# Optimization experiments

Hardware: AMD Instinct MI355X
Metric: run time of the kernel (lower is better)

The kernel has to match this reference:

```python
import jax, jax.numpy as jnp
import numpy as np

B, T_H, T_F = 8192, 128, 125
MOTION_DIM, H = 6, 128


def setup_inputs() -> dict:
    key = jax.random.key(0)
    ks = jax.random.split(key, 24)
    s = 1.0 / np.sqrt(H)  # torch LSTM/Linear default init scale

    def p(k, shape):
        return jax.random.uniform(k, shape, jnp.float32, -s, s)

    inp = {"hist": jax.random.normal(ks[0], (B, T_H, MOTION_DIM), jnp.float32)}
    i = 1
    for pre, in0 in (("enc", MOTION_DIM), ("dec", 2)):
        for l, ind in enumerate((in0, H)):
            inp[f"{pre}_Wih{l}"] = p(ks[i], (4 * H, ind)); i += 1
            inp[f"{pre}_Whh{l}"] = p(ks[i], (4 * H, H)); i += 1
            inp[f"{pre}_bih{l}"] = p(ks[i], (4 * H,)); i += 1
            inp[f"{pre}_bhh{l}"] = p(ks[i], (4 * H,)); i += 1
    inp["head_W1"] = p(ks[i], (128, H)); i += 1
    inp["head_b1"] = p(ks[i], (128,)); i += 1
    inp["head_W2"] = p(ks[i], (2, 128)); i += 1
    inp["head_b2"] = p(ks[i], (2,)); i += 1
    return inp


def _cell(x, h, c, Wih, Whh, bih, bhh):
    # PyTorch LSTM gate order: i, f, g, o
    gates = x @ Wih.T + h @ Whh.T + (bih + bhh)
    i, f, g, o = jnp.split(gates, 4, axis=-1)
    c = jax.nn.sigmoid(f) * c + jax.nn.sigmoid(i) * jnp.tanh(g)
    h = jax.nn.sigmoid(o) * jnpp_tanh(c) if False else jax.nn.sigmoid(o) * jnp.tanh(c)
    return h, c


def reference(hist,
              enc_Wih0, enc_Whh0, enc_bih0, enc_bhh0,
              enc_Wih1, enc_Whh1, enc_bih1, enc_bhh1,
              dec_Wih0, dec_Whh0, dec_bih0, dec_bhh0,
              dec_Wih1, dec_Whh1, dec_bih1, dec_bhh1,
              head_W1, head_b1, head_W2, head_b2):
    b = hist.shape[0]
    z = jnp.zeros((b, H), hist.dtype)

    # ---- encoder: 2-layer LSTM over hist, keep only final (h, c) ----
    def enc_step(carry, x_t):
        h0, c0, h1, c1 = carry
        h0, c0 = _cell(x_t, h0, c0, enc_Wih0, enc_Whh0, enc_bih0, enc_bhh0)
        h1, c1 = _cell(h0, h1, c1, enc_Wih1, enc_Whh1, enc_bih1, enc_bhh1)
        return (h0, c0, h1, c1), None

    (h0, c0, h1, c1), _ = jax.lax.scan(
        enc_step, (z, z, z, z), jnp.swapaxes(hist, 0, 1))  # [T_h, B, 6]

    last_pos = hist[:, -1, :2]

    def dec_step(carry, _):
        h0, c0, h1, c1, x = carry
        h0, c0 = _cell(x, h0, c0, dec_Wih0, dec_Whh0, dec_bih0, dec_bhh0)
        h1, c1 = _cell(h0, h1, c1, dec_Wih1, dec_Whh1, dec_bih1, dec_bhh1)
        nxt = jax.nn.relu(h1 @ head_W1.T + head_b1) @ head_W2.T + head_b2
        return (h0, c0, h1, c1, nxt), nxt

    _, preds = jax.lax.scan(dec_step, (h0, c0, h1, c1, last_pos), None,
                            length=T_F)
    return jnp.swapaxes(preds, 0, 1)  # [B, T_f, 2]
```

## Files before the change

### kernel.cpp

```cpp
#include <hip/hip_runtime.h>


typedef _Float16 f16;
typedef _Float16 f16x4 __attribute__((ext_vector_type(4)));
typedef _Float16 f16x8 __attribute__((ext_vector_type(8)));
typedef float    f32x4 __attribute__((ext_vector_type(4)));

#define MFMA16(a,b,c) __builtin_amdgcn_mfma_f32_16x16x32_f16((a),(b),(c),0,0,0)

#define BM 32
#define NBLK 256
#define PACE_TGT 32

#define HOFF_E0 0
#define HOFF_E1 81920
#define HOFF_D0 212992
#define HOFF_D1 294912
#define HOFF_H  425984
#define H_TOTAL 442368
#define FOFF    221184
#define FB_E0 0
#define FB_E1 512
#define FB_D0 1024
#define FB_D1 1536
#define FB_H1 2048
#define FB_W2 2176
#define FB_B2 2432
#define F_TOTAL 2434
#define BAR_F   2560
#define BAR_BYTES 8192

#define HS 140
#define XS 36
#define O1S 133

#define HBUF 4480
#define XBUF 1152
#define L_H0 0
#define L_H1 8960
#define L_XH 17920
#define L_XL 20224
#define L_HALVES 22528

__device__ __forceinline__ float fsig(float x){ return 1.0f/(1.0f+__expf(-x)); }
__device__ __forceinline__ float ftanh(float x){
  float a = fabsf(x);
  float e = __expf(-2.0f*a);
  float t = (1.0f-e)/(1.0f+e);
  return x < 0.0f ? -t : t;
}

__device__ __forceinline__ void grid_pace(unsigned* __restrict__ bar, int idx, int g, int tid){
  __syncthreads();
  if (tid == 0){
    unsigned* p = &bar[idx*8 + g];
    __hip_atomic_fetch_add(p, 1u, __ATOMIC_RELAXED, __HIP_MEMORY_SCOPE_AGENT);
    while (__hip_atomic_load(p, __ATOMIC_RELAXED, __HIP_MEMORY_SCOPE_AGENT) < (unsigned)PACE_TGT)
      __builtin_amdgcn_s_sleep(1);
  }
  __syncthreads();
}

template<int STRIDE>
__device__ __forceinline__ f16x8 load_afrag(const f16* buf, int m, int kc, int lane){
  const f16* p = buf + (m*16 + (lane&15))*STRIDE + kc + ((lane>>4)<<2);
  f16x4 lo = *(const f16x4*)p;
  f16x4 hi = *(const f16x4*)(p+16);
  return __builtin_shufflevector(lo, hi, 0,1,2,3,4,5,6,7);
}

__device__ __forceinline__ void init_acc(f32x4 acc[2][4],
                                         const float* __restrict__ bias, int wv, int lane){
#pragma unroll
  for (int i=0;i<4;++i){
    float bv = bias[i*128 + wv*16 + (lane&15)];
    f32x4 b4 = {bv,bv,bv,bv};
    acc[0][i]=b4; acc[1][i]=b4;
  }
}

template<int KT, int SPLIT, int SB, bool CLO>
__device__ __forceinline__ void gemm2(f32x4 acc[2][4],
    const f16x8* __restrict__ Bp,
    const f16* __restrict__ Ah,
    const f16* __restrict__ Ch, const f16* __restrict__ Cl,
    int wv, int lane)
{
  f16x8 Bc[4], Bn[4];
#pragma unroll
  for (int i=0;i<4;++i) Bc[i] = Bp[(i*8 + wv)*64 + lane];
#pragma unroll
  for (int kt=0; kt<KT; ++kt){
    if (kt+1 < KT){
#pragma unroll
      for (int i=0;i<4;++i) Bn[i] = Bp[((kt+1)*32 + i*8 + wv)*64 + lane];
    }
    if (kt < SPLIT){
      int kc = kt*32;
      f16x8 a0h = load_afrag<HS>(Ah, 0, kc, lane);
      f16x8 a1h = load_afrag<HS>(Ah, 1, kc, lane);
#pragma unroll
      for (int i=0;i<4;++i){
        acc[0][i] = MFMA16(a0h, Bc[i], acc[0][i]);
        acc[1][i] = MFMA16(a1h, Bc[i], acc[1][i]);
      }
    } else {
      int kc = (kt-SPLIT)*32;
      f16x8 c0h = load_afrag<SB>(Ch, 0, kc, lane);
      f16x8 c1h = load_afrag<SB>(Ch, 1, kc, lane);
#pragma unroll
      for (int i=0;i<4;++i){
        acc[0][i] = MFMA16(c0h, Bc[i], acc[0][i]);
        acc[1][i] = MFMA16(c1h, Bc[i], acc[1][i]);
      }
      if (CLO){
        f16x8 c0l = load_afrag<SB>(Cl, 0, kc, lane);
        f16x8 c1l = load_afrag<SB>(Cl, 1, kc, lane);
#pragma unroll
        for (int i=0;i<4;++i){
          acc[0][i] = MFMA16(c0l, Bc[i], acc[0][i]);
          acc[1][i] = MFMA16(c1l, Bc[i], acc[1][i]);
        }
      }
    }
#pragma unroll
    for (int i=0;i<4;++i) Bc[i] = Bn[i];
  }
}

__device__ __forceinline__ void lstm_update_m(f32x4 acc[2][4], float cr[2][4],
    f16* __restrict__ Dh, int wv, int lane)
{
  const int unit = wv*16 + (lane&15);
  const int rg   = (lane>>4)<<2;
#pragma unroll
  for (int mt=0;mt<2;++mt)
#pragma unroll
  for (int r=0;r<4;++r){
    float iv = fsig(acc[mt][0][r]);
    float fv = fsig(acc[mt][1][r]);
    float gv = ftanh(acc[mt][2][r]);
    float ov = fsig(acc[mt][3][r]);
    float cn = fv*cr[mt][r] + iv*gv;
    cr[mt][r] = cn;
    float h = ov*ftanh(cn);
    Dh[(mt*16 + rg + r)*HS + unit] = (f16)h;
  }
}

__global__ void __launch_bounds__(512, 2)
lstm_main(const float* __restrict__ hist, float* __restrict__ ws,
          float* __restrict__ out)
{
  const f16* wh = (const f16*)ws;
  const float* wf = ws + FOFF;
  unsigned* bar = (unsigned*)(ws + FOFF + BAR_F);
  const f16x8* BE0 = (const f16x8*)(wh + HOFF_E0);
  const f16x8* BE1 = (const f16x8*)(wh + HOFF_E1);
  const f16x8* BD0 = (const f16x8*)(wh + HOFF_D0);
  const f16x8* BD1 = (const f16x8*)(wh + HOFF_D1);
  const f16x8* BH  = (const f16x8*)(wh + HOFF_H);

  __shared__ __align__(16) f16 smem[L_HALVES];
  __shared__ __align__(16) float o1buf[32*O1S];

  const int tid  = threadIdx.x;
  const int wv   = tid >> 6;
  const int lane = tid & 63;
  const int b0   = blockIdx.x * BM;
  const int g    = blockIdx.x & 7;
  const int lidx = lane & 15;

  for (int i = tid; i < L_HALVES; i += 512) smem[i] = (f16)0.f;
  float c0r[2][4] = {{0,0,0,0},{0,0,0,0}};
  float c1r[2][4] = {{0,0,0,0},{0,0,0,0}};
  f32x4 acc[2][4];

  const int lr = tid/6, ld = tid - (tid/6)*6;

  __syncthreads();
  if (tid < 192){
    float v = hist[(b0+lr)*768 + ld];
    f16 hv = (f16)v;
    smem[L_XH + XBUF + lr*XS + ld] = hv;
    smem[L_XL + XBUF + lr*XS + ld] = (f16)(v - (float)hv);
  }
  __syncthreads();

  for (int t=0; t<128; ++t){
    const int c  = t & 1;
    const int hw = c*HBUF, hr = (c^1)*HBUF;
    const int xw = c*XBUF, xr = (c^1)*XBUF;

    init_acc(acc, wf + FB_E0, wv, lane);
    gemm2<5,4,XS,true>(acc, BE0,
                       smem + L_H0 + hr,
                       smem + L_XH + xr, smem + L_XL + xr, wv, lane);
    if (t < 127 && tid < 192){
      float v = hist[(b0+lr)*768 + (t+1)*6 + ld];
      f16 hv = (f16)v;
      smem[L_XH + xw + lr*XS + ld] = hv;
      smem[L_XL + xw + lr*XS + ld] = (f16)(v - (float)hv);
    }
    lstm_update_m(acc, c0r, smem + L_H0 + hw, wv, lane);
    __syncthreads();

    init_acc(acc, wf + FB_E1, wv, lane);
    gemm2<8,4,HS,false>(acc, BE1,
                        smem + L_H0 + hw,
                        smem + L_H1 + hr, smem + L_H1 + hr, wv, lane);
    lstm_update_m(acc, c1r, smem + L_H1 + hw, wv, lane);
    grid_pace(bar, t, g, tid);
  }

  if (tid < 64){
    int r = tid>>1, j = tid&1;
    float v = hist[(b0+r)*768 + 762 + j];
    f16 hv = (f16)v;
    smem[L_XH + XBUF + r*XS + j] = hv;
    smem[L_XL + XBUF + r*XS + j] = (f16)(v - (float)hv);
  }
  __syncthreads();

  for (int t=0; t<125; ++t){
    const int c  = t & 1;
    const int hw = c*HBUF, hr = (c^1)*HBUF;
    const int xw = c*XBUF, xr = (c^1)*XBUF;

    init_acc(acc, wf + FB_D0, wv, lane);
    gemm2<5,4,XS,true>(acc, BD0,
                       smem + L_H0 + hr,
                       smem + L_XH + xr, smem + L_XL + xr, wv, lane);
    lstm_update_m(acc, c0r, smem + L_H0 + hw, wv, lane);
    __syncthreads();

    init_acc(acc, wf + FB_D1, wv, lane);
    gemm2<8,4,HS,false>(acc, BD1,
                        smem + L_H0 + hw,
                        smem + L_H1 + hr, smem + L_H1 + hr, wv, lane);
    lstm_update_m(acc, c1r, smem + L_H1 + hw, wv, lane);
    __syncthreads();

    {
      const f16* h1wH = smem + L_H1 + hw;
      float bH1 = wf[FB_H1 + wv*16 + lidx];
      f32x4 ha0 = {bH1,bH1,bH1,bH1};
      f32x4 ha1 = ha0;
#pragma unroll
      for (int kt=0;kt<4;++kt){
        f16x8 Wc = BH[(kt*8 + wv)*64 + lane];
        int kc = kt*32;
        f16x8 a0h = load_afrag<HS>(h1wH, 0, kc, lane);
        f16x8 a1h = load_afrag<HS>(h1wH, 1, kc, lane);
        ha0 = MFMA16(a0h, Wc, ha0);
        ha1 = MFMA16(a1h, Wc, ha1);
      }
#pragma unroll
      for (int r=0;r<4;++r){
        float v0 = ha0[r]; v0 = v0 > 0.f ? v0 : 0.f;
        float v1 = ha1[r]; v1 = v1 > 0.f ? v1 : 0.f;
        int rr = ((lane>>4)<<2) + r;
        o1buf[rr*O1S      + wv*16 + lidx] = v0;
        o1buf[(16+rr)*O1S + wv*16 + lidx] = v1;
      }
    }
    __syncthreads();

    if (tid < 64){
      int r = tid>>1, j = tid&1;
      const float* op = o1buf + r*O1S;
      const float* w2 = wf + FB_W2 + j;
      float s0=0.f,s1=0.f,s2=0.f,s3=0.f;
#pragma unroll
      for (int k=0;k<128;k+=4){
        s0 = fmaf(op[k],   w2[2*k],   s0);
        s1 = fmaf(op[k+1], w2[2*k+2], s1);
        s2 = fmaf(op[k+2], w2[2*k+4], s2);
        s3 = fmaf(op[k+3], w2[2*k+6], s3);
      }
      float pred = wf[FB_B2 + j] + ((s0+s1)+(s2+s3));
      out[(b0+r)*250 + t*2 + j] = pred;
      f16 ph = (f16)pred;
      smem[L_XH + xw + r*XS + j] = ph;
      smem[L_XL + xw + r*XS + j] = (f16)(pred - (float)ph);
    }
    grid_pace(bar, 128 + t, g, tid);
  }
}

__global__ void setup_kernel(
    const float* __restrict__ eWih0, const float* __restrict__ eWhh0,
    const float* __restrict__ ebih0, const float* __restrict__ ebhh0,
    const float* __restrict__ eWih1, const float* __restrict__ eWhh1,
    const float* __restrict__ ebih1, const float* __restrict__ ebhh1,
    const float* __restrict__ dWih0, const float* __restrict__ dWhh0,
    const float* __restrict__ dbih0, const float* __restrict__ dbhh0,
    const float* __restrict__ dWih1, const float* __restrict__ dWhh1,
    const float* __restrict__ dbih1, const float* __restrict__ dbhh1,
    const float* __restrict__ W1, const float* __restrict__ b1,
    const float* __restrict__ W2, const float* __restrict__ b2,
    float* __restrict__ ws)
{
  int i = blockIdx.x*256 + threadIdx.x;
  if (i < H_TOTAL){
    f16* whp = (f16*)ws;
    const float *Wa, *Wb; int ka, kb, off; bool head = false;
    if      (i < HOFF_E1){ off=HOFF_E0; Wa=eWhh0; ka=128; Wb=eWih0; kb=6; }
    else if (i < HOFF_D0){ off=HOFF_E1; Wa=eWih1; ka=128; Wb=eWhh1; kb=128; }
    else if (i < HOFF_D1){ off=HOFF_D0; Wa=dWhh0; ka=128; Wb=dWih0; kb=2; }
    else if (i < HOFF_H) { off=HOFF_D1; Wa=dWih1; ka=128; Wb=dWhh1; kb=128; }
    else                 { off=HOFF_H;  Wa=W1; ka=128; Wb=W1; kb=0; head=true; }
    int local = i - off;
    int j     = local & 7;
    int lane  = (local>>3) & 63;
    int nk    = local >> 9;
    int NTl   = head ? 8 : 32;
    int n     = nk % NTl;
    int kt    = nk / NTl;
    int col   = n*16 + (lane&15);
    int koff  = ((j>>2)<<4) + ((lane>>4)<<2) + (j&3);
    int kin   = kt*32 + koff;
    float val;
    if (head){
      val = (kin < 128) ? W1[col*128 + kin] : 0.f;
    } else {
      val = (kin < ka) ? Wa[col*ka + kin]
          : ((kin < ka+kb) ? Wb[col*kb + (kin-ka)] : 0.f);
    }
    whp[i] = (f16)val;
  } else if (i < H_TOTAL + F_TOTAL){
    int f = i - H_TOTAL;
    float* wfp = ws + FOFF;
    if (f < 2048){
      int layer = f >> 9, c = f & 511;
      const float *bi, *bh;
      if      (layer==0){ bi=ebih0; bh=ebhh0; }
      else if (layer==1){ bi=ebih1; bh=ebhh1; }
      else if (layer==2){ bi=dbih0; bh=dbhh0; }
      else              { bi=dbih1; bh=dbhh1; }
      wfp[f] = bi[c] + bh[c];
    } else if (f < 2176){
      wfp[f] = b1[f-2048];
    } else if (f < 2432){
      int k = (f-2176)>>1, j = (f-2176)&1;
      wfp[f] = W2[j*128 + k];
    } else {
      wfp[f] = b2[f-2432];
    }
  }
}

extern "C" void kernel_launch(void* const* d_in, const int* in_sizes, int n_in,
                              void* d_out, int out_size, void* d_ws, size_t ws_size,
                              hipStream_t stream)
{
  const float* hist = (const float*)d_in[0];
  float* ws = (float*)d_ws;

  (void)hipMemsetAsync((char*)d_ws + (size_t)(FOFF + BAR_F)*4, 0, BAR_BYTES, stream);

  int total = H_TOTAL + F_TOTAL;
  setup_kernel<<<(total + 255)/256, 256, 0, stream>>>(
      (const float*)d_in[1],  (const float*)d_in[2],
      (const float*)d_in[3],  (const float*)d_in[4],
      (const float*)d_in[5],  (const float*)d_in[6],
      (const float*)d_in[7],  (const float*)d_in[8],
      (const float*)d_in[9],  (const float*)d_in[10],
      (const float*)d_in[11], (const float*)d_in[12],
      (const float*)d_in[13], (const float*)d_in[14],
      (const float*)d_in[15], (const float*)d_in[16],
      (const float*)d_in[17], (const float*)d_in[18],
      (const float*)d_in[19], (const float*)d_in[20],
      ws);

  lstm_main<<<NBLK, 512, 0, stream>>>(hist, ws, (float*)d_out);
}
```

Measured before the change: 2.916 ms.

## Pace grid every other step, pack barrier counters, parallelize head output dot

Grid pacing between blocks now runs only on odd timesteps in both the encoder and the decoder, halving the number of cross-block atomic spin barriers. Even steps use a plain block sync instead. The barrier counters are rearranged to group-major layout in a smaller buffer. The final 128-wide head dot product is spread over all threads with 8-way partial sums and shuffle reductions, where before 64 threads each ran a serial loop. The pacing only throttles skew between blocks for cache sharing, so fewer pace points lower sync overhead but may let blocks drift further apart.

```diff
diff --git a/kernel.cpp b/kernel.cpp
--- a/kernel.cpp
+++ b/kernel.cpp
@@ -28,7 +28,7 @@
 #define FB_B2 2432
 #define F_TOTAL 2434
 #define BAR_F   2560
-#define BAR_BYTES 8192
+#define BAR_BYTES 4096
 
 #define HS 140
 #define XS 36
@@ -53,7 +53,7 @@
 __device__ __forceinline__ void grid_pace(unsigned* __restrict__ bar, int idx, int g, int tid){
   __syncthreads();
   if (tid == 0){
-    unsigned* p = &bar[idx*8 + g];
+    unsigned* p = &bar[g*128 + idx];
     __hip_atomic_fetch_add(p, 1u, __ATOMIC_RELAXED, __HIP_MEMORY_SCOPE_AGENT);
     while (__hip_atomic_load(p, __ATOMIC_RELAXED, __HIP_MEMORY_SCOPE_AGENT) < (unsigned)PACE_TGT)
       __builtin_amdgcn_s_sleep(1);
@@ -210,9 +210,10 @@
                         smem + L_H0 + hw,
                         smem + L_H1 + hr, smem + L_H1 + hr, wv, lane);
     lstm_update_m(acc, c1r, smem + L_H1 + hw, wv, lane);
-    grid_pace(bar, t, g, tid);
-  }
-
+    if (t & 1) grid_pace(bar, t>>1, g, tid);
+  }
+
+  __syncthreads();
   if (tid < 64){
     int r = tid>>1, j = tid&1;
     float v = hist[(b0+r)*768 + 762 + j];
@@ -266,25 +267,32 @@
     }
     __syncthreads();
 
-    if (tid < 64){
-      int r = tid>>1, j = tid&1;
+    {
+      const int r = tid >> 4;
+      const int j = (tid >> 3) & 1;
+      const int s = tid & 7;
       const float* op = o1buf + r*O1S;
-      const float* w2 = wf + FB_W2 + j;
-      float s0=0.f,s1=0.f,s2=0.f,s3=0.f;
-#pragma unroll
-      for (int k=0;k<128;k+=4){
-        s0 = fmaf(op[k],   w2[2*k],   s0);
-        s1 = fmaf(op[k+1], w2[2*k+2], s1);
-        s2 = fmaf(op[k+2], w2[2*k+4], s2);
-        s3 = fmaf(op[k+3], w2[2*k+6], s3);
-      }
-      float pred = wf[FB_B2 + j] + ((s0+s1)+(s2+s3));
-      out[(b0+r)*250 + t*2 + j] = pred;
-      f16 ph = (f16)pred;
-      smem[L_XH + xw + r*XS + j] = ph;
-      smem[L_XL + xw + r*XS + j] = (f16)(pred - (float)ph);
-    }
-    grid_pace(bar, 128 + t, g, tid);
+      float pa=0.f, pb=0.f;
+#pragma unroll
+      for (int i=0;i<16;i+=2){
+        int k0 = i*8 + s, k1 = (i+1)*8 + s;
+        pa = fmaf(op[k0], wf[FB_W2 + k0*2 + j], pa);
+        pb = fmaf(op[k1], wf[FB_W2 + k1*2 + j], pb);
+      }
+      float p = pa + pb;
+      p += __shfl_xor(p, 1);
+      p += __shfl_xor(p, 2);
+      p += __shfl_xor(p, 4);
+      if (s == 0){
+        float pred = wf[FB_B2 + j] + p;
+        out[(b0+r)*250 + t*2 + j] = pred;
+        f16 ph = (f16)pred;
+        smem[L_XH + xw + r*XS + j] = ph;
+        smem[L_XL + xw + r*XS + j] = (f16)(pred - (float)ph);
+      }
+    }
+    if (t & 1) grid_pace(bar, 64 + (t>>1), g, tid);
+    else       __syncthreads();
   }
 }
 
```

After: 2.699 ms. 1.08x faster.
